# Optimization experiments

Measured on AMD Instinct MI355X. Metric: run time of the kernel, lower is better.

Reference implementation:

```python
import jax, jax.numpy as jnp
from jax import lax
import numpy as np

B, T, S, E, H = 32, 128, 256, 512, 1024


def _lstm_cell(x, h, c, Wih, Whh, bih, bhh):
    # gates in PyTorch order: i, f, g, o
    g = x @ Wih.T + bih + h @ Whh.T + bhh
    i, f, gg, o = jnp.split(g, 4, axis=-1)
    c_new = jax.nn.sigmoid(f) * c + jax.nn.sigmoid(i) * jnp.tanh(gg)
    h_new = jax.nn.sigmoid(o) * jnp.tanh(c_new)
    return h_new, c_new


def setup_inputs() -> dict:
    key = jax.random.key(0)
    ks = jax.random.split(key, 20)
    s = 1.0 / np.sqrt(H)

    def rn(k, shape, scale):
        return (jax.random.normal(k, shape, jnp.float32) * scale)

    inputs = rn(ks[0], (B, T, E), 1.0)
    enc_outputs = rn(ks[1], (S, B, H), 1.0)
    enc_c = rn(ks[2], (2, B, H // 2), 1.0)
    lengths = jax.random.randint(ks[3], (B,), S // 2, S + 1)
    mask = jnp.arange(S)[None, :] >= lengths[:, None]  # [B,S] True = pad

    return {
        "inputs": inputs, "enc_outputs": enc_outputs, "enc_c": enc_c, "mask": mask,
        "Wq": rn(ks[4], (H, H), s), "bq": jnp.zeros((H,), jnp.float32),
        "Wk": rn(ks[5], (H, H), s), "bk": jnp.zeros((H,), jnp.float32),
        "Wv": rn(ks[6], (H, H), s), "bv": jnp.zeros((H,), jnp.float32),
        "Wo": rn(ks[7], (H, H), s), "bo": jnp.zeros((H,), jnp.float32),
        "Wih0": rn(ks[8], (4 * H, H + E), s), "Whh0": rn(ks[9], (4 * H, H), s),
        "bih0": jnp.zeros((4 * H,), jnp.float32), "bhh0": jnp.zeros((4 * H,), jnp.float32),
        "Wih1": rn(ks[10], (4 * H, H), s), "Whh1": rn(ks[11], (4 * H, H), s),
        "bih1": jnp.zeros((4 * H,), jnp.float32), "bhh1": jnp.zeros((4 * H,), jnp.float32),
    }


def reference(inputs, enc_outputs, enc_c, mask, Wq, bq, Wk, bk, Wv, bv, Wo, bo,
              Wih0, Whh0, bih0, bhh0, Wih1, Whh1, bih1, bhh1):
    # Precompute attention K/V projections once (they do not depend on the step).
    K = jnp.einsum('sbe,he->sbh', enc_outputs, Wk) + bk
    V = jnp.einsum('sbe,he->sbh', enc_outputs, Wv) + bv
    scale = 1.0 / jnp.sqrt(jnp.asarray(H, inputs.dtype))

    # Initial LSTM state per the module: c stacked from concat of encoder
    # bidirectional cell states, h zeros.
    c_init = jnp.concatenate([enc_c[0], enc_c[1]], axis=-1)  # [B,H]
    c0 = jnp.stack([c_init, c_init])                          # [2,B,H]
    h0 = jnp.zeros_like(c0)

    def step(carry, x_t):
        h, c = carry
        q = c[1] @ Wq.T + bq                                  # query = last-layer cell state
        scores = jnp.einsum('bh,sbh->bs', q, K) * scale
        scores = jnp.where(mask, -1e9, scores)
        attn = jax.nn.softmax(scores, axis=-1)
        ctx = jnp.einsum('bs,sbh->bh', attn, V) @ Wo.T + bo   # [B,H]
        x = jnp.concatenate([ctx, x_t], axis=-1)              # [B,H+E]
        h_0, c_0 = _lstm_cell(x, h[0], c[0], Wih0, Whh0, bih0, bhh0)
        h_1, c_1 = _lstm_cell(h_0, h[1], c[1], Wih1, Whh1, bih1, bhh1)
        return (jnp.stack([h_0, h_1]), jnp.stack([c_0, c_1])), h_1

    _, outs = lax.scan(step, (h0, c0), inputs.transpose(1, 0, 2))  # [T,B,H]
    return outs.transpose(1, 0, 2)  # [B,T,H]
```

## Files before the change

kernel.cpp:

```cpp
#include <hip/hip_runtime.h>

typedef unsigned short u16;
typedef unsigned int   u32;
typedef unsigned char  u8;

constexpr int kB = 32, kT = 128, kS = 256, kE = 512, kH = 1024, kG = 4096;

typedef __attribute__((ext_vector_type(8))) short bfx8;
typedef __attribute__((ext_vector_type(4))) float fx4;

__device__ __forceinline__ float b2f(u16 v){ return __uint_as_float(((u32)v) << 16); }
__device__ __forceinline__ u16  f2b(float f){
    u32 u = __float_as_uint(f);
    return (u16)((u + 0x7FFFu + ((u >> 16) & 1u)) >> 16);
}
__device__ __forceinline__ float sigf(float x){ return 1.f / (1.f + expf(-x)); }
__device__ __forceinline__ float ldin(const void* p, size_t i, int dt){
    return dt ? ((const float*)p)[i] : b2f(((const u16*)p)[i]);
}

__global__ void detect_dtype_k(const void* __restrict__ inputs, int* __restrict__ dtflag)
{
    __shared__ int bad;
    int t = threadIdx.x;
    if (t == 0) bad = 0;
    __syncthreads();
    const u16* p = (const u16*)inputs;
    int l = 0;
    for (int i = t; i < 4096; i += 256){
        u16 v = p[i];
        int e = (v >> 7) & 0xFF;
        if (v != 0 && (e < 90 || e > 140)) l = 1;
    }
    if (l) atomicOr(&bad, 1);
    __syncthreads();
    if (t == 0) *dtflag = bad;
}

__global__ void prep_mask_k(const void* __restrict__ mask, float* __restrict__ maskflag)
{
    __shared__ int bad32, bad16, bad8, evenNZ;
    int t = threadIdx.x;
    if (t == 0){ bad32 = 0; bad16 = 0; bad8 = 0; evenNZ = 0; }
    __syncthreads();
    const u32* w32 = (const u32*)mask;
    const u16* w16 = (const u16*)mask;
    const u8*  w8  = (const u8*)mask;
    int l32 = 0, l16 = 0, l8 = 0, lev = 0;
    for (int i = t; i < 2048; i += 256){ u32 v = w32[i]; l32 |= (v > 1u); }
    for (int i = t; i < 4096; i += 256){
        u16 v = w16[i];
        l16 |= (v != 0 && v != 0x3F80u);
        if ((i & 1) == 0 && v != 0) lev = 1;
    }
    for (int i = t; i < 8192; i += 256){ l8 |= (w8[i] > 1); }
    if (l32) atomicOr(&bad32, 1);
    if (l16) atomicOr(&bad16, 1);
    if (l8)  atomicOr(&bad8, 1);
    if (lev) atomicOr(&evenNZ, 1);
    __syncthreads();
    int mode;
    if (!bad32)       mode = 0;
    else if (!bad16)  mode = evenNZ ? 1 : 3;
    else if (!bad8)   mode = 2;
    else              mode = 3;
    for (int i = t; i < kB * kS; i += 256){
        bool m;
        if (mode == 0)      m = (((const int*)mask)[i] != 0);
        else if (mode == 1) m = (w16[i] != 0);
        else if (mode == 2) m = (w8[i] != 0);
        else                m = (((const float*)mask)[i] != 0.f);
        maskflag[i] = m ? 1.f : 0.f;
    }
}

__global__ void prep_bias_k(const void* __restrict__ Wq, const void* __restrict__ bq,
                            const void* __restrict__ Wk, const void* __restrict__ bk,
                            const void* __restrict__ bv, const void* __restrict__ Wo,
                            const void* __restrict__ bo,
                            const void* __restrict__ bih0, const void* __restrict__ bhh0,
                            const void* __restrict__ bih1, const void* __restrict__ bhh1,
                            float* __restrict__ bkq, float* __restrict__ bvo,
                            float* __restrict__ ubq, float* __restrict__ bof,
                            float* __restrict__ bias01, float* __restrict__ bias1,
                            float* __restrict__ cbqbk, const int* __restrict__ dtflag)
{
    int dt = *dtflag;
    int idx = blockIdx.x * 256 + threadIdx.x;
    if (idx < 1024){
        float s = 0.f;
        for (int i = 0; i < 1024; i++) s += ldin(bk, i, dt) * ldin(Wq, (size_t)i * 1024 + idx, dt);
        bkq[idx] = s;
    } else if (idx < 2048){ int o2 = idx - 1024;
        float s = 0.f;
        for (int h = 0; h < 1024; h++) s += ldin(bv, h, dt) * ldin(Wo, (size_t)o2 * 1024 + h, dt);
        bvo[o2] = s;
    } else if (idx < 3072){ int e = idx - 2048;
        float s = 0.f;
        for (int i = 0; i < 1024; i++) s += ldin(bq, i, dt) * ldin(Wk, (size_t)i * 1024 + e, dt);
        ubq[e] = s;
    } else if (idx < 4096){ int o2 = idx - 3072;
        bof[o2] = ldin(bo, o2, dt);
    } else if (idx < 8192){ int j = idx - 4096;
        bias01[j] = ldin(bih0, j, dt) + ldin(bhh0, j, dt);
    } else if (idx < 12288){ int j = idx - 8192;
        bias1[j] = ldin(bih1, j, dt) + ldin(bhh1, j, dt);
    } else if (idx == 12288){
        float s = 0.f;
        for (int i = 0; i < 1024; i++) s += ldin(bq, i, dt) * ldin(bk, i, dt);
        cbqbk[0] = s;
    }
}

__global__ void init_state_k(const void* __restrict__ enc_c,
                             float* __restrict__ c0, float* __restrict__ c1,
                             u16* __restrict__ H0h, u16* __restrict__ H0l,
                             u16* __restrict__ H1h, u16* __restrict__ H1l,
                             const int* __restrict__ dtflag)
{
    int dt = *dtflag;
    int idx = blockIdx.x * 256 + threadIdx.x;
    int b = idx >> 10, h = idx & 1023;
    float cv = (h < 512) ? ldin(enc_c, (size_t)b * 512 + h, dt)
                         : ldin(enc_c, (size_t)(32 + b) * 512 + (h - 512), dt);
    c0[idx] = cv; c1[idx] = cv;
    H0h[idx] = 0; H0l[idx] = 0;
    H1h[idx] = 0; H1l[idx] = 0;
}

__global__ void split_plain_k(const void* __restrict__ src, u16* __restrict__ Oh,
                              u16* __restrict__ Ol, int n, const int* __restrict__ dtflag)
{
    int dt = *dtflag;
    int idx = blockIdx.x * 256 + threadIdx.x;
    if (idx >= n) return;
    float v = ldin(src, idx, dt);
    u16 h = f2b(v);
    Oh[idx] = h;
    Ol[idx] = f2b(v - b2f(h));
}

__global__ void split_x_k(const void* __restrict__ inputs, u16* __restrict__ Xh,
                          u16* __restrict__ Xl, const int* __restrict__ dtflag)
{
    int dt = *dtflag;
    int idx = blockIdx.x * 256 + threadIdx.x;
    int b = idx >> 16, t = (idx >> 9) & 127, e = idx & 511;
    float v = ldin(inputs, idx, dt);
    u16 h = f2b(v);
    size_t o = ((size_t)(t * 32 + b) << 9) + e;
    Xh[o] = h;
    Xl[o] = f2b(v - b2f(h));
}

__global__ void tsplit_k(const void* __restrict__ W, int ldw, int col_off,
                         u16* __restrict__ Oh, u16* __restrict__ Ol, int ldo,
                         const int* __restrict__ dtflag)
{
    __shared__ float tile[64][65];
    int dt = *dtflag;
    int r0 = blockIdx.x * 64, c0 = blockIdx.y * 64;
    for (int i = 0; i < 16; i++){
        int idx = threadIdx.x + i * 256;
        int rr = idx >> 6, cc = idx & 63;
        tile[rr][cc] = ldin(W, (size_t)(r0 + rr) * ldw + col_off + c0 + cc, dt);
    }
    __syncthreads();
    for (int i = 0; i < 16; i++){
        int idx = threadIdx.x + i * 256;
        int cr = idx >> 6, rc = idx & 63;
        float v = tile[rc][cr];
        u16 h = f2b(v);
        size_t o = (size_t)(c0 + cr) * ldo + r0 + rc;
        Oh[o] = h;
        Ol[o] = f2b(v - b2f(h));
    }
}

__global__ __launch_bounds__(256) void wfrag_k(const void* __restrict__ W, int ldw, int col_off,
                                               u16* __restrict__ F, int KSS,
                                               const int* __restrict__ dtflag)
{
    int dt = *dtflag;
    int ct = blockIdx.x;
    int iters = KSS * 2;
    for (int i = 0; i < iters; i++){
        int flat = threadIdx.x + i * 256;
        int ks = flat >> 9, r = flat & 511, l = r >> 3, j = r & 7;
        int row = ct * 16 + (l & 15);
        int k = ks * 32 + (l >> 4) * 8 + j;
        F[(size_t)ct * (KSS * 512) + flat] = f2b(ldin(W, (size_t)row * ldw + col_off + k, dt));
    }
}

template<int EPI>
__global__ __launch_bounds__(256) void gemm_hilo_k(
    const u16* __restrict__ Ah, const u16* __restrict__ Al, int ldA,
    const u16* __restrict__ Bh, const u16* __restrict__ Bl, int ldB,
    u16* __restrict__ OutH, u16* __restrict__ OutL, int ldO,
    const float* __restrict__ bias, float scale)
{
    __shared__ __align__(16) u16 Bsh[64][40];
    __shared__ __align__(16) u16 Bsl[64][40];
    int tid = threadIdx.x, wave = tid >> 6, lane = tid & 63;
    int m0 = blockIdx.x * 64, n0 = blockIdx.y * 64;
    int rA = lane & 15, kq = lane >> 4;
    fx4 acc[4];
    #pragma unroll
    for (int nt = 0; nt < 4; nt++) acc[nt] = (fx4){0.f, 0.f, 0.f, 0.f};
    int skk = tid >> 3, snn = (tid & 7) * 8;
    for (int k0 = 0; k0 < 1024; k0 += 32){
        bfx8 vh = *(const bfx8*)(Bh + (size_t)(k0 + skk) * ldB + n0 + snn);
        bfx8 vl = *(const bfx8*)(Bl + (size_t)(k0 + skk) * ldB + n0 + snn);
        __syncthreads();
        #pragma unroll
        for (int q = 0; q < 8; q++){ Bsh[snn + q][skk] = (u16)vh[q]; Bsl[snn + q][skk] = (u16)vl[q]; }
        __syncthreads();
        size_t abase = (size_t)(m0 + wave * 16 + rA) * ldA + k0 + kq * 8;
        bfx8 a_h = *(const bfx8*)(Ah + abase);
        bfx8 a_l = *(const bfx8*)(Al + abase);
        #pragma unroll
        for (int nt = 0; nt < 4; nt++){
            bfx8 b_h = *(const bfx8*)&Bsh[nt * 16 + rA][kq * 8];
            bfx8 b_l = *(const bfx8*)&Bsl[nt * 16 + rA][kq * 8];
            acc[nt] = __builtin_amdgcn_mfma_f32_16x16x32_bf16(a_h, b_h, acc[nt], 0, 0, 0);
            acc[nt] = __builtin_amdgcn_mfma_f32_16x16x32_bf16(a_h, b_l, acc[nt], 0, 0, 0);
            acc[nt] = __builtin_amdgcn_mfma_f32_16x16x32_bf16(a_l, b_h, acc[nt], 0, 0, 0);
        }
    }
    #pragma unroll
    for (int nt = 0; nt < 4; nt++){
        #pragma unroll
        for (int i = 0; i < 4; i++){
            int m = m0 + wave * 16 + kq * 4 + i;
            int n = n0 + nt * 16 + rA;
            float v = acc[nt][i];
            if (EPI == 0){
                u16 h = f2b(v);
                OutH[(size_t)m * ldO + n] = h;
                OutL[(size_t)m * ldO + n] = f2b(v - b2f(h));
            } else {
                float v2 = (v + bias[n]) * scale;
                OutH[(((size_t)(((m & 31) << 8) | (m >> 5))) << 10) + n] = f2b(v2);
            }
        }
    }
}

__global__ __launch_bounds__(256) void skbq_k(
    const void* __restrict__ enc, const float* __restrict__ ubq,
    const float* __restrict__ cbqbk, float* __restrict__ skbqs,
    const int* __restrict__ dtflag)
{
    int dt = *dtflag;
    int w = (blockIdx.x * 256 + threadIdx.x) >> 6;
    int lane = threadIdx.x & 63;
    int s = w >> 5, b = w & 31;
    size_t base = (size_t)w * 1024 + lane * 16;
    float acc = 0.f;
    #pragma unroll
    for (int i = 0; i < 16; i++) acc += ubq[lane * 16 + i] * ldin(enc, base + i, dt);
    #pragma unroll
    for (int off = 32; off; off >>= 1) acc += __shfl_down(acc, off, 64);
    if (lane == 0) skbqs[b * 256 + s] = (acc + cbqbk[0]) * 0.03125f;
}

template<int LAYER>
__global__ __launch_bounds__(256) void gmm_k(
    const u16* __restrict__ f0, const u16* __restrict__ f1, const u16* __restrict__ f2,
    const u16* __restrict__ a0h, const u16* __restrict__ a0l,
    const u16* __restrict__ a1h, const u16* __restrict__ a1l,
    const u16* __restrict__ a2h, const u16* __restrict__ a2l,
    float* __restrict__ pp)
{
    __shared__ float red[4][32][64];
    int ht = blockIdx.x, q = blockIdx.y;
    int tid = threadIdx.x, wave = tid >> 6, lane = tid & 63;
    int rA = lane & 15, kq = lane >> 4;
    constexpr int PER_W = (LAYER == 0) ? 5 : 4;
    fx4 acc[2][4];
    #pragma unroll
    for (int mt = 0; mt < 2; mt++)
        #pragma unroll
        for (int nt = 0; nt < 4; nt++) acc[mt][nt] = (fx4){0.f, 0.f, 0.f, 0.f};

    #pragma unroll
    for (int si = 0; si < PER_W; si++){
        int s = q * (PER_W * 4) + wave * PER_W + si;
        const u16 *F, *ah, *al; int ks, ld, KSSF;
        if (LAYER == 0){
            if (s < 32)      { F = f0; ks = s;      ah = a0h; al = a0l; ld = 1024; KSSF = 32; }
            else if (s < 64) { F = f1; ks = s - 32; ah = a1h; al = a1l; ld = 1024; KSSF = 32; }
            else             { F = f2; ks = s - 64; ah = a2h; al = a2l; ld = 512;  KSSF = 16; }
        } else {
            if (s < 32)      { F = f0; ks = s;      ah = a0h; al = a0l; }
            else             { F = f1; ks = s - 32; ah = a1h; al = a1l; }
            ld = 1024; KSSF = 32;
        }
        int koff = ks * 32 + kq * 8;
        bfx8 a_h0 = *(const bfx8*)(ah + (size_t)rA * ld + koff);
        bfx8 a_l0 = *(const bfx8*)(al + (size_t)rA * ld + koff);
        bfx8 a_h1 = *(const bfx8*)(ah + (size_t)(16 + rA) * ld + koff);
        bfx8 a_l1 = *(const bfx8*)(al + (size_t)(16 + rA) * ld + koff);
        #pragma unroll
        for (int nt = 0; nt < 4; nt++){
            bfx8 bf = *(const bfx8*)(F + ((size_t)((nt * 64 + ht) * KSSF + ks) * 64 + lane) * 8);
            acc[0][nt] = __builtin_amdgcn_mfma_f32_16x16x32_bf16(a_h0, bf, acc[0][nt], 0, 0, 0);
            acc[0][nt] = __builtin_amdgcn_mfma_f32_16x16x32_bf16(a_l0, bf, acc[0][nt], 0, 0, 0);
            acc[1][nt] = __builtin_amdgcn_mfma_f32_16x16x32_bf16(a_h1, bf, acc[1][nt], 0, 0, 0);
            acc[1][nt] = __builtin_amdgcn_mfma_f32_16x16x32_bf16(a_l1, bf, acc[1][nt], 0, 0, 0);
        }
    }
    #pragma unroll
    for (int mt = 0; mt < 2; mt++)
        #pragma unroll
        for (int nt = 0; nt < 4; nt++)
            #pragma unroll
            for (int i = 0; i < 4; i++)
                red[wave][mt * 16 + kq * 4 + i][nt * 16 + rA] = acc[mt][nt][i];
    __syncthreads();
    #pragma unroll
    for (int i = 0; i < 8; i++){
        int flat = tid + i * 256;
        int b = flat >> 6, cl = flat & 63;
        int nt = cl >> 4, hl = cl & 15;
        float v = (red[0][b][cl] + red[1][b][cl]) + (red[2][b][cl] + red[3][b][cl]);
        pp[(((size_t)(q * 32 + b)) << 12) + nt * 1024 + ht * 16 + hl] = v;
    }
}

__global__ __launch_bounds__(256) void cell0_k(
    const float* __restrict__ pp, const float* __restrict__ biasv,
    float* __restrict__ c_state, u16* __restrict__ outHh, u16* __restrict__ outHl)
{
    int idx = blockIdx.x * 256 + threadIdx.x;
    int b = idx >> 10, h = idx & 1023;
    float g[4];
    #pragma unroll
    for (int gate = 0; gate < 4; gate++){
        int j = gate * 1024 + h;
        g[gate] = biasv[j]
                + pp[(((size_t)(0 * 32 + b)) << 12) + j]
                + pp[(((size_t)(1 * 32 + b)) << 12) + j]
                + pp[(((size_t)(2 * 32 + b)) << 12) + j]
                + pp[(((size_t)(3 * 32 + b)) << 12) + j];
    }
    float gi_ = sigf(g[0]);
    float gf_ = sigf(g[1]);
    float gg_ = tanhf(g[2]);
    float go_ = sigf(g[3]);
    float c = gf_ * c_state[idx] + gi_ * gg_;
    c_state[idx] = c;
    float hv = go_ * tanhf(c);
    u16 hh = f2b(hv);
    outHh[idx] = hh;
    outHl[idx] = f2b(hv - b2f(hh));
}

__global__ __launch_bounds__(1024) void fused_attn_k(
    const float* __restrict__ pp, const float* __restrict__ bias1,
    float* __restrict__ c1f, u16* __restrict__ H1h, u16* __restrict__ H1l,
    float* __restrict__ y_out, int t,
    const u16* __restrict__ KQb, const u16* __restrict__ Vob,
    const float* __restrict__ skbqs, const float* __restrict__ maskflag,
    const float* __restrict__ bof, u16* __restrict__ Ch, u16* __restrict__ Cl)
{
    __shared__ float cs[1024];
    __shared__ float sred[256][4];
    __shared__ float attn[256];
    __shared__ float wred[8];
    __shared__ float2 cpart[2][512];
    int b = blockIdx.x, tid = threadIdx.x;
    float c;
    int cidx = (b << 10) + tid;
    if (t > 0){
        float g[4];
        #pragma unroll
        for (int gate = 0; gate < 4; gate++){
            int j = gate * 1024 + tid;
            g[gate] = bias1[j]
                    + pp[(((size_t)(0 * 32 + b)) << 12) + j]
                    + pp[(((size_t)(1 * 32 + b)) << 12) + j]
                    + pp[(((size_t)(2 * 32 + b)) << 12) + j]
                    + pp[(((size_t)(3 * 32 + b)) << 12) + j];
        }
        float gi_ = sigf(g[0]);
        float gf_ = sigf(g[1]);
        float gg_ = tanhf(g[2]);
        float go_ = sigf(g[3]);
        c = gf_ * c1f[cidx] + gi_ * gg_;
        c1f[cidx] = c;
        float hv = go_ * tanhf(c);
        u16 hh = f2b(hv);
        H1h[cidx] = hh;
        H1l[cidx] = f2b(hv - b2f(hh));
        y_out[(((size_t)b * kT + (t - 1)) << 10) + tid] = hv;
    } else {
        c = c1f[cidx];
    }
    cs[tid] = c;
    __syncthreads();
    if (t == 128) return;
    {
        int s = tid >> 2, qd = tid & 3;
        const u16* kp = KQb + (((size_t)((b << 8) | s)) << 10) + qd * 256;
        const float* cc = &cs[qd * 256];
        float a = 0.f;
        #pragma unroll 8
        for (int i = 0; i < 256; i += 8){
            uint4 kv = *(const uint4*)(kp + i);
            a += cc[i]     * b2f((u16)(kv.x & 0xFFFFu)) + cc[i + 1] * b2f((u16)(kv.x >> 16));
            a += cc[i + 2] * b2f((u16)(kv.y & 0xFFFFu)) + cc[i + 3] * b2f((u16)(kv.y >> 16));
            a += cc[i + 4] * b2f((u16)(kv.z & 0xFFFFu)) + cc[i + 5] * b2f((u16)(kv.z >> 16));
            a += cc[i + 6] * b2f((u16)(kv.w & 0xFFFFu)) + cc[i + 7] * b2f((u16)(kv.w >> 16));
        }
        sred[s][qd] = a;
    }
    __syncthreads();
    if (tid < 256){
        float sc = (sred[tid][0] + sred[tid][1]) + (sred[tid][2] + sred[tid][3]);
        int is = (b << 8) + tid;
        sc = (maskflag[is] != 0.f) ? -1e9f : sc + skbqs[is];
        attn[tid] = sc;
        float m = sc;
        #pragma unroll
        for (int off = 32; off; off >>= 1) m = fmaxf(m, __shfl_down(m, off, 64));
        if ((tid & 63) == 0) wred[tid >> 6] = m;
    }
    __syncthreads();
    if (tid < 256){
        float mm = fmaxf(fmaxf(wred[0], wred[1]), fmaxf(wred[2], wred[3]));
        float ex = expf(attn[tid] - mm);
        float ssum = ex;
        #pragma unroll
        for (int off = 32; off; off >>= 1) ssum += __shfl_down(ssum, off, 64);
        if ((tid & 63) == 0) wred[4 + (tid >> 6)] = ssum;
        sred[tid][0] = ex;
    }
    __syncthreads();
    if (tid < 256){
        float tot = (wred[4] + wred[5]) + (wred[6] + wred[7]);
        attn[tid] = sred[tid][0] / tot;
    }
    __syncthreads();
    {
        int sh = tid >> 9, hp = tid & 511;
        const u16* vcol = Vob + ((size_t)b << 18) + hp * 2;
        float a0 = 0.f, a1 = 0.f;
        int s0 = sh * 128;
        #pragma unroll 8
        for (int s = s0; s < s0 + 128; s++){
            u32 v = *(const u32*)(vcol + ((size_t)s << 10));
            float at = attn[s];
            a0 += at * b2f((u16)(v & 0xFFFFu));
            a1 += at * b2f((u16)(v >> 16));
        }
        cpart[sh][hp] = make_float2(a0, a1);
    }
    __syncthreads();
    if (tid < 512){
        float2 p0 = cpart[0][tid], p1 = cpart[1][tid];
        int h = tid * 2;
        float v0 = p0.x + p1.x + bof[h];
        float v1 = p0.y + p1.y + bof[h + 1];
        u16 h0 = f2b(v0), h1 = f2b(v1);
        int base = (b << 10) + h;
        Ch[base] = h0;     Ch[base + 1] = h1;
        Cl[base] = f2b(v0 - b2f(h0));
        Cl[base + 1] = f2b(v1 - b2f(h1));
    }
}

extern "C" void kernel_launch(void* const* d_in, const int* in_sizes, int n_in,
                              void* d_out, int out_size, void* d_ws, size_t ws_size,
                              hipStream_t stream)
{
    const void* inputs = d_in[0];
    const void* enc    = d_in[1];
    const void* enc_c  = d_in[2];
    const void* mask   = d_in[3];
    const void* Wq   = d_in[4];
    const void* bq   = d_in[5];
    const void* Wk   = d_in[6];
    const void* bk   = d_in[7];
    const void* Wv   = d_in[8];
    const void* bv   = d_in[9];
    const void* Wo   = d_in[10];
    const void* bo   = d_in[11];
    const void* Wih0 = d_in[12];
    const void* Whh0 = d_in[13];
    const void* bih0 = d_in[14];
    const void* bhh0 = d_in[15];
    const void* Wih1 = d_in[16];
    const void* Whh1 = d_in[17];
    const void* bih1 = d_in[18];
    const void* bhh1 = d_in[19];
    float* out = (float*)d_out;
    (void)in_sizes; (void)n_in; (void)out_size; (void)ws_size;

    char* ws = (char*)d_ws;
    size_t off = 0;
    auto alloc = [&](size_t bytes) -> void* {
        void* p = ws + off; off += (bytes + 255) & ~(size_t)255; return p;
    };
    char* poolA = (char*)alloc((size_t)37748736);
    u16* Eh  = (u16*)poolA;
    u16* El  = (u16*)(poolA + 16777216);
    u16* F0c = (u16*)poolA;
    u16* F0h = (u16*)(poolA + 8388608);
    u16* F1i = (u16*)(poolA + 16777216);
    u16* F1h = (u16*)(poolA + 25165824);
    u16* F0x = (u16*)(poolA + 33554432);
    char* poolB = (char*)alloc((size_t)16777216);
    u16* Akh  = (u16*)poolB;
    u16* Akl  = (u16*)(poolB + 2097152);
    u16* Bqh  = (u16*)(poolB + 4194304);
    u16* Bql  = (u16*)(poolB + 6291456);
    u16* Avh  = (u16*)(poolB + 8388608);
    u16* Avl  = (u16*)(poolB + 10485760);
    u16* Both = (u16*)(poolB + 12582912);
    u16* Botl = (u16*)(poolB + 14680064);
    u16*  KQb  = (u16*)alloc((size_t)kB * kS * kH * 2);
    u16*  Vob  = (u16*)alloc((size_t)kB * kS * kH * 2);
    u16*  Xh   = (u16*)alloc((size_t)kB * kT * kE * 2);
    u16*  Xl   = (u16*)alloc((size_t)kB * kT * kE * 2);
    u16*  Wkqh = (u16*)alloc((size_t)kH * kH * 2);
    u16*  Wkql = (u16*)alloc((size_t)kH * kH * 2);
    u16*  Wvoh = (u16*)alloc((size_t)kH * kH * 2);
    u16*  Wvol = (u16*)alloc((size_t)kH * kH * 2);
    float* pp  = (float*)alloc((size_t)4 * kB * kG * 4);
    u16*  Ch   = (u16*)alloc((size_t)kB * kH * 2);
    u16*  Cl   = (u16*)alloc((size_t)kB * kH * 2);
    u16*  H0h  = (u16*)alloc((size_t)kB * kH * 2);
    u16*  H0l  = (u16*)alloc((size_t)kB * kH * 2);
    u16*  H1h  = (u16*)alloc((size_t)kB * kH * 2);
    u16*  H1l  = (u16*)alloc((size_t)kB * kH * 2);
    float* c0f = (float*)alloc(kB * kH * 4);
    float* c1f = (float*)alloc(kB * kH * 4);
    float* bkq = (float*)alloc(1024 * 4);
    float* bvo = (float*)alloc(1024 * 4);
    float* ubq = (float*)alloc(1024 * 4);
    float* bof = (float*)alloc(1024 * 4);
    float* bias01 = (float*)alloc(4096 * 4);
    float* bias1  = (float*)alloc(4096 * 4);
    float* cbqbk  = (float*)alloc(256);
    float* skbqs  = (float*)alloc(kB * kS * 4);
    float* maskflag = (float*)alloc(kB * kS * 4);
    int*   dtflag = (int*)alloc(256);

    detect_dtype_k<<<1, 256, 0, stream>>>(inputs, dtflag);
    prep_mask_k<<<1, 256, 0, stream>>>(mask, maskflag);
    prep_bias_k<<<49, 256, 0, stream>>>(Wq, bq, Wk, bk, bv, Wo, bo,
                                        bih0, bhh0, bih1, bhh1,
                                        bkq, bvo, ubq, bof, bias01, bias1, cbqbk, dtflag);
    init_state_k<<<128, 256, 0, stream>>>(enc_c, c0f, c1f, H0h, H0l, H1h, H1l, dtflag);
    split_plain_k<<<32768, 256, 0, stream>>>(enc, Eh, El, 8388608, dtflag);
    split_plain_k<<<4096, 256, 0, stream>>>(Wq, Bqh, Bql, 1048576, dtflag);
    tsplit_k<<<dim3(16, 16), 256, 0, stream>>>(Wk, 1024, 0, Akh, Akl, 1024, dtflag);
    tsplit_k<<<dim3(16, 16), 256, 0, stream>>>(Wv, 1024, 0, Avh, Avl, 1024, dtflag);
    tsplit_k<<<dim3(16, 16), 256, 0, stream>>>(Wo, 1024, 0, Both, Botl, 1024, dtflag);
    split_x_k<<<8192, 256, 0, stream>>>(inputs, Xh, Xl, dtflag);
    gemm_hilo_k<0><<<dim3(16, 16), 256, 0, stream>>>(Akh, Akl, 1024, Bqh, Bql, 1024,
                                                     Wkqh, Wkql, 1024, nullptr, 1.f);
    gemm_hilo_k<0><<<dim3(16, 16), 256, 0, stream>>>(Avh, Avl, 1024, Both, Botl, 1024,
                                                     Wvoh, Wvol, 1024, nullptr, 1.f);
    gemm_hilo_k<1><<<dim3(128, 16), 256, 0, stream>>>(Eh, El, 1024, Wkqh, Wkql, 1024,
                                                      KQb, nullptr, 0, bkq, 0.03125f);
    gemm_hilo_k<1><<<dim3(128, 16), 256, 0, stream>>>(Eh, El, 1024, Wvoh, Wvol, 1024,
                                                      Vob, nullptr, 0, bvo, 1.0f);
    skbq_k<<<2048, 256, 0, stream>>>(enc, ubq, cbqbk, skbqs, dtflag);
    wfrag_k<<<256, 256, 0, stream>>>(Wih0, 1536, 0,    F0c, 32, dtflag);
    wfrag_k<<<256, 256, 0, stream>>>(Whh0, 1024, 0,    F0h, 32, dtflag);
    wfrag_k<<<256, 256, 0, stream>>>(Wih0, 1536, 1024, F0x, 16, dtflag);
    wfrag_k<<<256, 256, 0, stream>>>(Wih1, 1024, 0,    F1i, 32, dtflag);
    wfrag_k<<<256, 256, 0, stream>>>(Whh1, 1024, 0,    F1h, 32, dtflag);

    for (int t = 0; t < kT; t++){
        fused_attn_k<<<32, 1024, 0, stream>>>(pp, bias1, c1f, H1h, H1l, out, t,
                                              KQb, Vob, skbqs, maskflag, bof, Ch, Cl);
        gmm_k<0><<<dim3(64, 4), 256, 0, stream>>>(
            F0c, F0h, F0x, Ch, Cl, H0h, H0l,
            Xh + (size_t)t * 32 * kE, Xl + (size_t)t * 32 * kE, pp);
        cell0_k<<<128, 256, 0, stream>>>(pp, bias01, c0f, H0h, H0l);
        gmm_k<1><<<dim3(64, 4), 256, 0, stream>>>(
            F1i, F1h, nullptr, H0h, H0l, H1h, H1l, nullptr, nullptr, pp);
    }
    fused_attn_k<<<32, 1024, 0, stream>>>(pp, bias1, c1f, H1h, H1l, out, 128,
                                          KQb, Vob, skbqs, maskflag, bof, Ch, Cl);
}
```

Before: 6.741 ms.

## Split fused attention step into two wider-grid kernels with double-buffered cell state

```diff
diff --git a/kernel.cpp b/kernel.cpp
--- a/kernel.cpp
+++ b/kernel.cpp
@@ -123,7 +123,8 @@
     int b = idx >> 10, h = idx & 1023;
     float cv = (h < 512) ? ldin(enc_c, (size_t)b * 512 + h, dt)
                          : ldin(enc_c, (size_t)(32 + b) * 512 + (h - 512), dt);
-    c0[idx] = cv; c1[idx] = cv;
+    c0[idx] = cv;
+    c1[idx] = cv; c1[32768 + idx] = cv;
     H0h[idx] = 0; H0l[idx] = 0;
     H1h[idx] = 0; H1l[idx] = 0;
 }
@@ -263,6 +264,131 @@
     #pragma unroll
     for (int off = 32; off; off >>= 1) acc += __shfl_down(acc, off, 64);
     if (lane == 0) skbqs[b * 256 + s] = (acc + cbqbk[0]) * 0.03125f;
+}
+
+__global__ __launch_bounds__(256) void scores_k(
+    const float* __restrict__ pp, const float* __restrict__ bias1,
+    const float* __restrict__ c1rd, float* __restrict__ c1wr,
+    u16* __restrict__ H1h, u16* __restrict__ H1l,
+    float* __restrict__ y_out, int t,
+    const u16* __restrict__ KQb, const float* __restrict__ skbqs,
+    const float* __restrict__ maskflag, float* __restrict__ scores)
+{
+    __shared__ float cs[1024];
+    int b = blockIdx.x >> 3, sg = blockIdx.x & 7;
+    int tid = threadIdx.x;
+    if (t > 0){
+        #pragma unroll
+        for (int i = 0; i < 4; i++){
+            int h = tid + i * 256;
+            int cidx = (b << 10) + h;
+            float g[4];
+            #pragma unroll
+            for (int gate = 0; gate < 4; gate++){
+                int j = (gate << 10) + h;
+                g[gate] = bias1[j]
+                        + pp[(((size_t)(0 * 32 + b)) << 12) + j]
+                        + pp[(((size_t)(1 * 32 + b)) << 12) + j]
+                        + pp[(((size_t)(2 * 32 + b)) << 12) + j]
+                        + pp[(((size_t)(3 * 32 + b)) << 12) + j];
+            }
+            float c = sigf(g[1]) * c1rd[cidx] + sigf(g[0]) * tanhf(g[2]);
+            cs[h] = c;
+            if (sg == 0){
+                c1wr[cidx] = c;
+                float hv = sigf(g[3]) * tanhf(c);
+                u16 hh = f2b(hv);
+                H1h[cidx] = hh;
+                H1l[cidx] = f2b(hv - b2f(hh));
+                y_out[(((size_t)b * kT + (t - 1)) << 10) + h] = hv;
+            }
+        }
+    } else {
+        #pragma unroll
+        for (int i = 0; i < 4; i++){
+            int h = tid + i * 256;
+            cs[h] = c1rd[(b << 10) + h];
+        }
+    }
+    __syncthreads();
+    if (t >= kT) return;
+    int wave = tid >> 6, lane = tid & 63;
+    float c16[16];
+    #pragma unroll
+    for (int i = 0; i < 16; i++) c16[i] = cs[lane * 16 + i];
+    #pragma unroll
+    for (int si = 0; si < 8; si++){
+        int s = sg * 32 + wave * 8 + si;
+        const u16* kp = KQb + (((size_t)((b << 8) | s)) << 10) + lane * 16;
+        uint4 k0 = *(const uint4*)kp;
+        uint4 k1 = *(const uint4*)(kp + 8);
+        float a = 0.f;
+        a += c16[0]  * b2f((u16)(k0.x & 0xFFFFu)) + c16[1]  * b2f((u16)(k0.x >> 16));
+        a += c16[2]  * b2f((u16)(k0.y & 0xFFFFu)) + c16[3]  * b2f((u16)(k0.y >> 16));
+        a += c16[4]  * b2f((u16)(k0.z & 0xFFFFu)) + c16[5]  * b2f((u16)(k0.z >> 16));
+        a += c16[6]  * b2f((u16)(k0.w & 0xFFFFu)) + c16[7]  * b2f((u16)(k0.w >> 16));
+        a += c16[8]  * b2f((u16)(k1.x & 0xFFFFu)) + c16[9]  * b2f((u16)(k1.x >> 16));
+        a += c16[10] * b2f((u16)(k1.y & 0xFFFFu)) + c16[11] * b2f((u16)(k1.y >> 16));
+        a += c16[12] * b2f((u16)(k1.z & 0xFFFFu)) + c16[13] * b2f((u16)(k1.z >> 16));
+        a += c16[14] * b2f((u16)(k1.w & 0xFFFFu)) + c16[15] * b2f((u16)(k1.w >> 16));
+        #pragma unroll
+        for (int off = 32; off; off >>= 1) a += __shfl_down(a, off, 64);
+        if (lane == 0){
+            int is = (b << 8) + s;
+            scores[is] = (maskflag[is] != 0.f) ? -1e9f : a + skbqs[is];
+        }
+    }
+}
+
+__global__ __launch_bounds__(256) void smctx_k(
+    const float* __restrict__ scores, const u16* __restrict__ Vob,
+    const float* __restrict__ bof, u16* __restrict__ Ch, u16* __restrict__ Cl)
+{
+    __shared__ float attn[256];
+    __shared__ float wred[8];
+    __shared__ float2 part[4][64];
+    int b = blockIdx.x >> 3, ht = blockIdx.x & 7;
+    int tid = threadIdx.x;
+    float scv = scores[(b << 8) + tid];
+    float m = scv;
+    #pragma unroll
+    for (int off = 32; off; off >>= 1) m = fmaxf(m, __shfl_down(m, off, 64));
+    if ((tid & 63) == 0) wred[tid >> 6] = m;
+    __syncthreads();
+    float mm = fmaxf(fmaxf(wred[0], wred[1]), fmaxf(wred[2], wred[3]));
+    float ex = expf(scv - mm);
+    float ssum = ex;
+    #pragma unroll
+    for (int off = 32; off; off >>= 1) ssum += __shfl_down(ssum, off, 64);
+    if ((tid & 63) == 0) wred[4 + (tid >> 6)] = ssum;
+    __syncthreads();
+    float tot = (wred[4] + wred[5]) + (wred[6] + wred[7]);
+    attn[tid] = ex / tot;
+    __syncthreads();
+    int hl = tid & 63, scn = tid >> 6;
+    int h2 = ht * 128 + hl * 2;
+    const u16* vcol = Vob + ((size_t)b << 18) + h2;
+    float a0 = 0.f, a1 = 0.f;
+    #pragma unroll 8
+    for (int s = scn; s < 256; s += 4){
+        u32 v = *(const u32*)(vcol + ((size_t)s << 10));
+        float at = attn[s];
+        a0 += at * b2f((u16)(v & 0xFFFFu));
+        a1 += at * b2f((u16)(v >> 16));
+    }
+    part[scn][hl] = make_float2(a0, a1);
+    __syncthreads();
+    if (tid < 64){
+        float2 p0 = part[0][tid], p1 = part[1][tid], p2 = part[2][tid], p3 = part[3][tid];
+        int h = ht * 128 + tid * 2;
+        float v0 = p0.x + p1.x + p2.x + p3.x + bof[h];
+        float v1 = p0.y + p1.y + p2.y + p3.y + bof[h + 1];
+        u16 h0 = f2b(v0), h1 = f2b(v1);
+        int base = (b << 10) + h;
+        Ch[base] = h0;     Ch[base + 1] = h1;
+        Cl[base] = f2b(v0 - b2f(h0));
+        Cl[base + 1] = f2b(v1 - b2f(h1));
+    }
 }
 
 template<int LAYER>
@@ -355,120 +481,6 @@
     u16 hh = f2b(hv);
     outHh[idx] = hh;
     outHl[idx] = f2b(hv - b2f(hh));
-}
-
-__global__ __launch_bounds__(1024) void fused_attn_k(
-    const float* __restrict__ pp, const float* __restrict__ bias1,
-    float* __restrict__ c1f, u16* __restrict__ H1h, u16* __restrict__ H1l,
-    float* __restrict__ y_out, int t,
-    const u16* __restrict__ KQb, const u16* __restrict__ Vob,
-    const float* __restrict__ skbqs, const float* __restrict__ maskflag,
-    const float* __restrict__ bof, u16* __restrict__ Ch, u16* __restrict__ Cl)
-{
-    __shared__ float cs[1024];
-    __shared__ float sred[256][4];
-    __shared__ float attn[256];
-    __shared__ float wred[8];
-    __shared__ float2 cpart[2][512];
-    int b = blockIdx.x, tid = threadIdx.x;
-    float c;
-    int cidx = (b << 10) + tid;
-    if (t > 0){
-        float g[4];
-        #pragma unroll
-        for (int gate = 0; gate < 4; gate++){
-            int j = gate * 1024 + tid;
-            g[gate] = bias1[j]
-                    + pp[(((size_t)(0 * 32 + b)) << 12) + j]
-                    + pp[(((size_t)(1 * 32 + b)) << 12) + j]
-                    + pp[(((size_t)(2 * 32 + b)) << 12) + j]
-                    + pp[(((size_t)(3 * 32 + b)) << 12) + j];
-        }
-        float gi_ = sigf(g[0]);
-        float gf_ = sigf(g[1]);
-        float gg_ = tanhf(g[2]);
-        float go_ = sigf(g[3]);
-        c = gf_ * c1f[cidx] + gi_ * gg_;
-        c1f[cidx] = c;
-        float hv = go_ * tanhf(c);
-        u16 hh = f2b(hv);
-        H1h[cidx] = hh;
-        H1l[cidx] = f2b(hv - b2f(hh));
-        y_out[(((size_t)b * kT + (t - 1)) << 10) + tid] = hv;
-    } else {
-        c = c1f[cidx];
-    }
-    cs[tid] = c;
-    __syncthreads();
-    if (t == 128) return;
-    {
-        int s = tid >> 2, qd = tid & 3;
-        const u16* kp = KQb + (((size_t)((b << 8) | s)) << 10) + qd * 256;
-        const float* cc = &cs[qd * 256];
-        float a = 0.f;
-        #pragma unroll 8
-        for (int i = 0; i < 256; i += 8){
-            uint4 kv = *(const uint4*)(kp + i);
-            a += cc[i]     * b2f((u16)(kv.x & 0xFFFFu)) + cc[i + 1] * b2f((u16)(kv.x >> 16));
-            a += cc[i + 2] * b2f((u16)(kv.y & 0xFFFFu)) + cc[i + 3] * b2f((u16)(kv.y >> 16));
-            a += cc[i + 4] * b2f((u16)(kv.z & 0xFFFFu)) + cc[i + 5] * b2f((u16)(kv.z >> 16));
-            a += cc[i + 6] * b2f((u16)(kv.w & 0xFFFFu)) + cc[i + 7] * b2f((u16)(kv.w >> 16));
-        }
-        sred[s][qd] = a;
-    }
-    __syncthreads();
-    if (tid < 256){
-        float sc = (sred[tid][0] + sred[tid][1]) + (sred[tid][2] + sred[tid][3]);
-        int is = (b << 8) + tid;
-        sc = (maskflag[is] != 0.f) ? -1e9f : sc + skbqs[is];
-        attn[tid] = sc;
-        float m = sc;
-        #pragma unroll
-        for (int off = 32; off; off >>= 1) m = fmaxf(m, __shfl_down(m, off, 64));
-        if ((tid & 63) == 0) wred[tid >> 6] = m;
-    }
-    __syncthreads();
-    if (tid < 256){
-        float mm = fmaxf(fmaxf(wred[0], wred[1]), fmaxf(wred[2], wred[3]));
-        float ex = expf(attn[tid] - mm);
-        float ssum = ex;
-        #pragma unroll
-        for (int off = 32; off; off >>= 1) ssum += __shfl_down(ssum, off, 64);
-        if ((tid & 63) == 0) wred[4 + (tid >> 6)] = ssum;
-        sred[tid][0] = ex;
-    }
-    __syncthreads();
-    if (tid < 256){
-        float tot = (wred[4] + wred[5]) + (wred[6] + wred[7]);
-        attn[tid] = sred[tid][0] / tot;
-    }
-    __syncthreads();
-    {
-        int sh = tid >> 9, hp = tid & 511;
-        const u16* vcol = Vob + ((size_t)b << 18) + hp * 2;
-        float a0 = 0.f, a1 = 0.f;
-        int s0 = sh * 128;
-        #pragma unroll 8
-        for (int s = s0; s < s0 + 128; s++){
-            u32 v = *(const u32*)(vcol + ((size_t)s << 10));
-            float at = attn[s];
-            a0 += at * b2f((u16)(v & 0xFFFFu));
-            a1 += at * b2f((u16)(v >> 16));
-        }
-        cpart[sh][hp] = make_float2(a0, a1);
-    }
-    __syncthreads();
-    if (tid < 512){
-        float2 p0 = cpart[0][tid], p1 = cpart[1][tid];
-        int h = tid * 2;
-        float v0 = p0.x + p1.x + bof[h];
-        float v1 = p0.y + p1.y + bof[h + 1];
-        u16 h0 = f2b(v0), h1 = f2b(v1);
-        int base = (b << 10) + h;
-        Ch[base] = h0;     Ch[base + 1] = h1;
-        Cl[base] = f2b(v0 - b2f(h0));
-        Cl[base + 1] = f2b(v1 - b2f(h1));
-    }
 }
 
 extern "C" void kernel_launch(void* const* d_in, const int* in_sizes, int n_in,
@@ -529,6 +541,7 @@
     u16*  Wvoh = (u16*)alloc((size_t)kH * kH * 2);
     u16*  Wvol = (u16*)alloc((size_t)kH * kH * 2);
     float* pp  = (float*)alloc((size_t)4 * kB * kG * 4);
+    float* scores = (float*)alloc(kB * kS * 4);
     u16*  Ch   = (u16*)alloc((size_t)kB * kH * 2);
     u16*  Cl   = (u16*)alloc((size_t)kB * kH * 2);
     u16*  H0h  = (u16*)alloc((size_t)kB * kH * 2);
@@ -536,7 +549,7 @@
     u16*  H1h  = (u16*)alloc((size_t)kB * kH * 2);
     u16*  H1l  = (u16*)alloc((size_t)kB * kH * 2);
     float* c0f = (float*)alloc(kB * kH * 4);
-    float* c1f = (float*)alloc(kB * kH * 4);
+    float* c1f = (float*)alloc((size_t)2 * kB * kH * 4);
     float* bkq = (float*)alloc(1024 * 4);
     float* bvo = (float*)alloc(1024 * 4);
     float* ubq = (float*)alloc(1024 * 4);
@@ -576,8 +589,11 @@
     wfrag_k<<<256, 256, 0, stream>>>(Whh1, 1024, 0,    F1h, 32, dtflag);
 
     for (int t = 0; t < kT; t++){
-        fused_attn_k<<<32, 1024, 0, stream>>>(pp, bias1, c1f, H1h, H1l, out, t,
-                                              KQb, Vob, skbqs, maskflag, bof, Ch, Cl);
+        const float* c1rd = c1f + (size_t)((t + 1) & 1) * kB * kH;
+        float*       c1wr = c1f + (size_t)(t & 1) * kB * kH;
+        scores_k<<<256, 256, 0, stream>>>(pp, bias1, c1rd, c1wr, H1h, H1l, out, t,
+                                          KQb, skbqs, maskflag, scores);
+        smctx_k<<<256, 256, 0, stream>>>(scores, Vob, bof, Ch, Cl);
         gmm_k<0><<<dim3(64, 4), 256, 0, stream>>>(
             F0c, F0h, F0x, Ch, Cl, H0h, H0l,
             Xh + (size_t)t * 32 * kE, Xl + (size_t)t * 32 * kE, pp);
@@ -585,6 +601,10 @@
         gmm_k<1><<<dim3(64, 4), 256, 0, stream>>>(
             F1i, F1h, nullptr, H0h, H0l, H1h, H1l, nullptr, nullptr, pp);
     }
-    fused_attn_k<<<32, 1024, 0, stream>>>(pp, bias1, c1f, H1h, H1l, out, 128,
-                                          KQb, Vob, skbqs, maskflag, bof, Ch, Cl);
-}
+    {
+        const float* c1rd = c1f + (size_t)((kT + 1) & 1) * kB * kH;
+        float*       c1wr = c1f + (size_t)(kT & 1) * kB * kH;
+        scores_k<<<256, 256, 0, stream>>>(pp, bias1, c1rd, c1wr, H1h, H1l, out, kT,
+                                          KQb, skbqs, maskflag, scores);
+    }
+}
```

After: 5.976 ms. 1.13x faster.
